# Performance work log

Hardware: AMD Instinct MI355X
Metric: run time of the kernel (lower is better)

## Reference

```python
import jax, jax.numpy as jnp
import numpy as np

B, N, D, H = 8, 1024, 1024, 16
DH = D // H
EPS = 1e-5


def setup_inputs() -> dict:
    key = jax.random.key(0)
    ks = jax.random.split(key, 12)
    s = 0.02
    return {
        "k": jax.random.normal(ks[0], (B, N, D), jnp.float32),
        "q": jax.random.normal(ks[1], (B, N, D), jnp.float32),
        "r": jax.random.normal(ks[2], (B, N, D), jnp.float32),
        "Wk": jax.random.normal(ks[3], (D, D), jnp.float32) * s,
        "bk": jnp.zeros((D,), jnp.float32),
        "Wq": jax.random.normal(ks[4], (D, D), jnp.float32) * s,
        "bq": jnp.zeros((D,), jnp.float32),
        "Wv": jax.random.normal(ks[5], (D, D), jnp.float32) * s,
        "bv": jnp.zeros((D,), jnp.float32),
        "Wo": jax.random.normal(ks[6], (D, D), jnp.float32) * s,
        "bo": jnp.zeros((D,), jnp.float32),
        "g1": jnp.ones((D,), jnp.float32),
        "b1": jnp.zeros((D,), jnp.float32),
        "g2": jnp.ones((D,), jnp.float32),
        "b2": jnp.zeros((D,), jnp.float32),
    }


def _layer_norm(x, g, b):
    mu = jnp.mean(x, axis=-1, keepdims=True)
    var = jnp.mean(jnp.square(x - mu), axis=-1, keepdims=True)
    return (x - mu) * jax.lax.rsqrt(var + EPS) * g + b


def reference(k, q, r, Wk, bk, Wq, bq, Wv, bv, Wo, bo, g1, b1, g2, b2):
    # linear projections (torch Linear: x @ W.T + b)
    kh = (k @ Wk.T + bk).reshape(B, -1, H, DH).transpose(0, 2, 1, 3)  # [B,H,Nk,DH]
    qh = (q @ Wq.T + bq).reshape(B, -1, H, DH).transpose(0, 2, 1, 3)  # [B,H,Nq,DH]
    vh = (r @ Wv.T + bv).reshape(B, -1, H, DH).transpose(0, 2, 1, 3)  # [B,H,Nk,DH]
    scale = 1.0 / jnp.sqrt(jnp.float32(DH))
    scores = jnp.einsum('bhid,bhjd->bhij', qh, kh) * scale  # [B,H,Nq,Nk]
    attn = jax.nn.softmax(scores, axis=-1)
    o = jnp.einsum('bhij,bhjd->bhid', attn, vh)  # [B,H,Nq,DH]
    o = o.transpose(0, 2, 1, 3).reshape(B, -1, D)
    mha = o @ Wo.T + bo
    residual = _layer_norm(mha + q, g1, b1)
    # source bug: mlp = nn.ReLU(BatchLinear(...)) -> mlp is plain ReLU
    out = _layer_norm(jax.nn.relu(residual) + residual, g2, b2)
    return out
```

## Files before the change

kernel.cpp:

```cpp
#include <hip/hip_runtime.h>
#include <hip/hip_bf16.h>
#include <math.h>

#define BB 8
#define NN 1024
#define DD 1024
#define HH 16
#define DH 64
#define MTOK 8192

typedef __attribute__((ext_vector_type(8))) short short8;
typedef __attribute__((ext_vector_type(4))) short short4v;
typedef __attribute__((ext_vector_type(4))) float float4v;

__device__ __forceinline__ ushort f2bf(float f) {
    union { float f; unsigned u; } v; v.f = f;
    unsigned r = v.u + 0x7fffu + ((v.u >> 16) & 1u);
    return (ushort)(r >> 16);
}

__device__ __forceinline__ void gl_lds16(const ushort* g, ushort* l) {
    __builtin_amdgcn_global_load_lds(
        (const __attribute__((address_space(1))) void*)g,
        (__attribute__((address_space(3))) void*)l, 16, 0, 0);
}

__device__ __forceinline__ void stage8f(const float* __restrict__ p, ushort* d) {
    float4v a = *(const float4v*)p;
    float4v b = *(const float4v*)(p + 4);
    short8 s;
    s[0]=(short)f2bf(a[0]); s[1]=(short)f2bf(a[1]); s[2]=(short)f2bf(a[2]); s[3]=(short)f2bf(a[3]);
    s[4]=(short)f2bf(b[0]); s[5]=(short)f2bf(b[1]); s[6]=(short)f2bf(b[2]); s[7]=(short)f2bf(b[3]);
    *(short8*)d = s;
}

struct CvtArgs {
    const float* src[7];
    ushort* dst[7];
    int n[7];
};
__global__ __launch_bounds__(256) void cvt_bf16(CvtArgs a) {
    const int z = blockIdx.y;
    const int idx = (blockIdx.x * 256 + threadIdx.x) * 8;
    if (idx >= a.n[z]) return;
    const float* s = a.src[z];
    float4v x0 = *(const float4v*)(s + idx);
    float4v x1 = *(const float4v*)(s + idx + 4);
    short8 o;
    o[0]=(short)f2bf(x0[0]); o[1]=(short)f2bf(x0[1]); o[2]=(short)f2bf(x0[2]); o[3]=(short)f2bf(x0[3]);
    o[4]=(short)f2bf(x1[0]); o[5]=(short)f2bf(x1[1]); o[6]=(short)f2bf(x1[2]); o[7]=(short)f2bf(x1[3]);
    *(short8*)(a.dst[z] + idx) = o;
}

template <typename TA, typename TW, int MODE>
__device__ __forceinline__ void gemm_core(const void* Ap, const void* Wp,
                                          const float* __restrict__ bias,
                                          void* __restrict__ outp,
                                          ushort* As, ushort* Bs) {
    constexpr bool A_BF = (sizeof(TA) == 2);
    constexpr bool W_BF = (sizeof(TW) == 2);
    constexpr int LDA = A_BF ? 64 : 72;
    constexpr int LDB = W_BF ? 64 : 72;

    const int tid  = threadIdx.x;
    const int wid  = tid >> 6;
    const int lane = tid & 63;
    const int quad = lane >> 4;
    const int l15  = lane & 15;
    const int wr   = wid >> 1;
    const int wc   = wid & 1;
    const int m0   = blockIdx.x * 128;
    const int n0   = blockIdx.y * 128;
    const int sw   = l15 & 7;

    float4v acc[4][4] = {};

    for (int kt = 0; kt < 16; ++kt) {
        const int k0 = kt * 64;
        if constexpr (A_BF) {
            const ushort* A = (const ushort*)Ap;
            #pragma unroll
            for (int t = 0; t < 4; ++t) {
                int chunk = t * 4 + wid;
                int row   = chunk * 8 + (lane >> 3);
                int kc    = ((lane & 7) ^ (lane >> 3)) * 8;
                gl_lds16(A + (size_t)(m0 + row) * 1024 + k0 + kc, As + chunk * 512);
            }
        } else {
            const float* A = (const float*)Ap;
            #pragma unroll
            for (int i = 0; i < 4; ++i) {
                int cidx = i * 256 + tid;
                int row  = cidx >> 3;
                int kc   = (cidx & 7) * 8;
                stage8f(A + (size_t)(m0 + row) * 1024 + k0 + kc, &As[row * 72 + kc]);
            }
        }
        if constexpr (W_BF) {
            const ushort* W = (const ushort*)Wp;
            #pragma unroll
            for (int t = 0; t < 4; ++t) {
                int chunk = t * 4 + wid;
                int row   = chunk * 8 + (lane >> 3);
                int kc    = ((lane & 7) ^ (lane >> 3)) * 8;
                gl_lds16(W + (size_t)(n0 + row) * 1024 + k0 + kc, Bs + chunk * 512);
            }
        } else {
            const float* W = (const float*)Wp;
            #pragma unroll
            for (int i = 0; i < 4; ++i) {
                int cidx = i * 256 + tid;
                int row  = cidx >> 3;
                int kc   = (cidx & 7) * 8;
                stage8f(W + (size_t)(n0 + row) * 1024 + k0 + kc, &Bs[row * 72 + kc]);
            }
        }
        __syncthreads();

        #pragma unroll
        for (int kk = 0; kk < 2; ++kk) {
            short8 af[4], bfr[4];
            #pragma unroll
            for (int i = 0; i < 4; ++i)
                af[i] = *(const short8*)&As[(wr * 64 + i * 16 + l15) * LDA +
                        (A_BF ? (((kk * 4 + quad) ^ sw) * 8) : (kk * 32 + quad * 8))];
            #pragma unroll
            for (int j = 0; j < 4; ++j)
                bfr[j] = *(const short8*)&Bs[(wc * 64 + j * 16 + l15) * LDB +
                         (W_BF ? (((kk * 4 + quad) ^ sw) * 8) : (kk * 32 + quad * 8))];
            #pragma unroll
            for (int i = 0; i < 4; ++i)
                #pragma unroll
                for (int j = 0; j < 4; ++j) {
                    if constexpr (MODE == 1)
                        acc[i][j] = __builtin_amdgcn_mfma_f32_16x16x32_bf16(af[i], bfr[j], acc[i][j], 0, 0, 0);
                    else
                        acc[j][i] = __builtin_amdgcn_mfma_f32_16x16x32_bf16(bfr[j], af[i], acc[j][i], 0, 0, 0);
                }
        }
        __syncthreads();
    }

    if constexpr (MODE == 1) {
        ushort* out = (ushort*)outp;
        #pragma unroll
        for (int j = 0; j < 4; ++j) {
            const int col = n0 + wc * 64 + j * 16 + l15;
            const float bv = bias[col];
            const int h = col >> 6;
            const int d = col & 63;
            #pragma unroll
            for (int i = 0; i < 4; ++i) {
                const int rowbase = m0 + wr * 64 + i * 16 + quad * 4;
                int bi = rowbase >> 10, n = rowbase & 1023;
                short4v pk;
                #pragma unroll
                for (int r = 0; r < 4; ++r) pk[r] = (short)f2bf(acc[i][j][r] + bv);
                *(short4v*)&out[(((size_t)(bi * HH + h) * DH + d) * NN) + n] = pk;
            }
        }
    } else {
        #pragma unroll
        for (int p = 0; p < 4; ++p) {
            const int fb = n0 + wc * 64 + p * 16 + quad * 4;
            const float4v bv4 = *(const float4v*)&bias[fb];
            const int h = fb >> 6;
            const int d = fb & 63;
            #pragma unroll
            for (int q = 0; q < 4; ++q) {
                const int tok = m0 + wr * 64 + q * 16 + l15;
                if constexpr (MODE == 0) {
                    ushort* out = (ushort*)outp;
                    int bi = tok >> 10, n = tok & 1023;
                    short4v pk;
                    #pragma unroll
                    for (int r = 0; r < 4; ++r) pk[r] = (short)f2bf(acc[p][q][r] + bv4[r]);
                    *(short4v*)&out[(((size_t)(bi * HH + h) * NN + n) * DH) + d] = pk;
                } else {
                    float* out = (float*)outp;
                    float4v ov;
                    #pragma unroll
                    for (int r = 0; r < 4; ++r) ov[r] = acc[p][q][r] + bv4[r];
                    *(float4v*)&out[(size_t)tok * 1024 + fb] = ov;
                }
            }
        }
    }
}

template <typename TA, typename TW>
__global__ __launch_bounds__(256) void proj3(const void* q, const void* k, const void* r,
                                             const void* Wq, const void* Wk, const void* Wv,
                                             const float* bq, const float* bk, const float* bv,
                                             ushort* qh, ushort* kh, ushort* vt) {
    constexpr int SA = (sizeof(TA) == 2) ? 64 : 72;
    constexpr int SB = (sizeof(TW) == 2) ? 64 : 72;
    __shared__ ushort As[128 * SA];
    __shared__ ushort Bs[128 * SB];
    if (blockIdx.z == 0)      gemm_core<TA, TW, 0>(q, Wq, bq, qh, As, Bs);
    else if (blockIdx.z == 1) gemm_core<TA, TW, 0>(k, Wk, bk, kh, As, Bs);
    else                      gemm_core<TA, TW, 1>(r, Wv, bv, vt, As, Bs);
}

template <typename TA, typename TW>
__global__ __launch_bounds__(256) void gemm_out(const void* A, const void* W,
                                                const float* bias, float* out) {
    constexpr int SA = (sizeof(TA) == 2) ? 64 : 72;
    constexpr int SB = (sizeof(TW) == 2) ? 64 : 72;
    __shared__ ushort As[128 * SA];
    __shared__ ushort Bs[128 * SB];
    gemm_core<TA, TW, 2>(A, W, bias, out, As, Bs);
}

__global__ __launch_bounds__(256) void attn_fused(const ushort* __restrict__ qh,
                                                  const ushort* __restrict__ kh,
                                                  const ushort* __restrict__ vt,
                                                  ushort* __restrict__ o) {
    __shared__ ushort Ks[64 * 64];
    __shared__ ushort Vs[64 * 64];
    __shared__ ushort Ps[4][2][16 * 72];

    const int tid  = threadIdx.x;
    const int wid  = tid >> 6;
    const int lane = tid & 63;
    const int quad = lane >> 4;
    const int l15  = lane & 15;
    const int sw   = l15 & 7;
    const int bh   = blockIdx.x;
    const int qt   = blockIdx.y;
    const int h    = bh & 15;
    const int b    = bh >> 4;

    const ushort* qb = qh + (size_t)bh * NN * DH;
    const ushort* kb = kh + (size_t)bh * NN * DH;
    const ushort* vb = vt + (size_t)bh * DH * NN;

    short8 qf[2][2];
    #pragma unroll
    for (int u = 0; u < 2; ++u) {
        const int qrow = qt * 128 + wid * 32 + u * 16 + l15;
        qf[u][0] = *(const short8*)(qb + (size_t)qrow * DH + quad * 8);
        qf[u][1] = *(const short8*)(qb + (size_t)qrow * DH + 32 + quad * 8);
    }

    float lsum[2] = {0.f, 0.f};
    float4v oaccT[2][4] = {};
    const float SCL = 0.18033688011f;

    for (int kt = 0; kt < 16; ++kt) {
        #pragma unroll
        for (int t = 0; t < 2; ++t) {
            int chunk = t * 4 + wid;
            int row   = chunk * 8 + (lane >> 3);
            int kc    = ((lane & 7) ^ (lane >> 3)) * 8;
            gl_lds16(kb + (size_t)(kt * 64 + row) * DH + kc, Ks + chunk * 512);
            gl_lds16(vb + (size_t)row * NN + kt * 64 + kc, Vs + chunk * 512);
        }
        __syncthreads();

        float4v sacc[2][4] = {};
        #pragma unroll
        for (int s = 0; s < 2; ++s)
            #pragma unroll
            for (int c = 0; c < 4; ++c) {
                short8 kf = *(const short8*)&Ks[(c * 16 + l15) * 64 + ((s * 4 + quad) ^ sw) * 8];
                #pragma unroll
                for (int u = 0; u < 2; ++u)
                    sacc[u][c] = __builtin_amdgcn_mfma_f32_16x16x32_bf16(kf, qf[u][s], sacc[u][c], 0, 0, 0);
            }

        #pragma unroll
        for (int u = 0; u < 2; ++u)
            #pragma unroll
            for (int c = 0; c < 4; ++c) {
                short4v pk;
                #pragma unroll
                for (int rr = 0; rr < 4; ++rr) {
                    float p = exp2f(sacc[u][c][rr] * SCL);
                    lsum[u] += p;
                    pk[rr] = (short)f2bf(p);
                }
                *(short4v*)&Ps[wid][u][l15 * 72 + c * 16 + quad * 4] = pk;
            }

        #pragma unroll
        for (int s = 0; s < 2; ++s) {
            short8 pf[2];
            #pragma unroll
            for (int u = 0; u < 2; ++u)
                pf[u] = *(const short8*)&Ps[wid][u][l15 * 72 + s * 32 + quad * 8];
            #pragma unroll
            for (int nn = 0; nn < 4; ++nn) {
                short8 vf = *(const short8*)&Vs[(nn * 16 + l15) * 64 + ((s * 4 + quad) ^ sw) * 8];
                #pragma unroll
                for (int u = 0; u < 2; ++u)
                    oaccT[u][nn] = __builtin_amdgcn_mfma_f32_16x16x32_bf16(vf, pf[u], oaccT[u][nn], 0, 0, 0);
            }
        }
        __syncthreads();
    }

    #pragma unroll
    for (int u = 0; u < 2; ++u) {
        float t = lsum[u];
        t += __shfl_xor(t, 16);
        t += __shfl_xor(t, 32);
        float inv = 1.0f / t;
        int row = qt * 128 + wid * 32 + u * 16 + l15;
        size_t base = ((size_t)b * NN + row) * DD + h * 64 + quad * 4;
        #pragma unroll
        for (int nn = 0; nn < 4; ++nn) {
            short4v pk;
            #pragma unroll
            for (int rr = 0; rr < 4; ++rr) pk[rr] = (short)f2bf(oaccT[u][nn][rr] * inv);
            *(short4v*)&o[base + nn * 16] = pk;
        }
    }
}

__global__ __launch_bounds__(256) void ln_fuse(const float* __restrict__ mha,
                                               const float* __restrict__ q,
                                               const float* __restrict__ g1,
                                               const float* __restrict__ b1,
                                               const float* __restrict__ g2,
                                               const float* __restrict__ b2,
                                               float* __restrict__ out) {
    __shared__ float red1[8];
    __shared__ float red2[8];
    const int tid  = threadIdx.x;
    const int wid  = tid >> 6;
    const int lane = tid & 63;
    const size_t base = (size_t)blockIdx.x * 1024 + tid * 4;

    float4v xv = *(const float4v*)(mha + base);
    float4v qv = *(const float4v*)(q + base);
    float x[4];
    float s = 0.f, ss = 0.f;
    for (int i = 0; i < 4; ++i) {
        x[i] = xv[i] + qv[i];
        s += x[i]; ss += x[i] * x[i];
    }
    for (int off = 1; off < 64; off <<= 1) {
        s += __shfl_xor(s, off); ss += __shfl_xor(ss, off);
    }
    if (lane == 0) { red1[wid * 2] = s; red1[wid * 2 + 1] = ss; }
    __syncthreads();
    s  = red1[0] + red1[2] + red1[4] + red1[6];
    ss = red1[1] + red1[3] + red1[5] + red1[7];
    float mu = s * (1.0f / 1024.0f);
    float rstd = rsqrtf(ss * (1.0f / 1024.0f) - mu * mu + 1e-5f);

    float4v g1v = *(const float4v*)(g1 + tid * 4);
    float4v b1v = *(const float4v*)(b1 + tid * 4);
    float y[4];
    float s2 = 0.f, ss2 = 0.f;
    for (int i = 0; i < 4; ++i) {
        float rr = (x[i] - mu) * rstd * g1v[i] + b1v[i];
        y[i] = fmaxf(rr, 0.f) + rr;
        s2 += y[i]; ss2 += y[i] * y[i];
    }
    for (int off = 1; off < 64; off <<= 1) {
        s2 += __shfl_xor(s2, off); ss2 += __shfl_xor(ss2, off);
    }
    if (lane == 0) { red2[wid * 2] = s2; red2[wid * 2 + 1] = ss2; }
    __syncthreads();
    s2  = red2[0] + red2[2] + red2[4] + red2[6];
    ss2 = red2[1] + red2[3] + red2[5] + red2[7];
    float mu2 = s2 * (1.0f / 1024.0f);
    float rstd2 = rsqrtf(ss2 * (1.0f / 1024.0f) - mu2 * mu2 + 1e-5f);

    float4v g2v = *(const float4v*)(g2 + tid * 4);
    float4v b2v = *(const float4v*)(b2 + tid * 4);
    float4v ov;
    for (int i = 0; i < 4; ++i) ov[i] = (y[i] - mu2) * rstd2 * g2v[i] + b2v[i];
    *(float4v*)(out + base) = ov;
}

extern "C" void kernel_launch(void* const* d_in, const int* in_sizes, int n_in,
                              void* d_out, int out_size, void* d_ws, size_t ws_size,
                              hipStream_t stream) {
    const float* k  = (const float*)d_in[0];
    const float* q  = (const float*)d_in[1];
    const float* r  = (const float*)d_in[2];
    const float* Wk = (const float*)d_in[3];
    const float* bk = (const float*)d_in[4];
    const float* Wq = (const float*)d_in[5];
    const float* bq = (const float*)d_in[6];
    const float* Wv = (const float*)d_in[7];
    const float* bv = (const float*)d_in[8];
    const float* Wo = (const float*)d_in[9];
    const float* bo = (const float*)d_in[10];
    const float* g1 = (const float*)d_in[11];
    const float* b1 = (const float*)d_in[12];
    const float* g2 = (const float*)d_in[13];
    const float* b2 = (const float*)d_in[14];

    char* ws = (char*)d_ws;
    const size_t MB = 1u << 20;
    dim3 blk(256);

    if (ws_size >= 121 * MB) {
        ushort* qc  = (ushort*)(ws);
        ushort* kc  = (ushort*)(ws + 16 * MB);
        ushort* rc  = (ushort*)(ws + 32 * MB);
        ushort* Wqc = (ushort*)(ws + 48 * MB);
        ushort* Wkc = (ushort*)(ws + 50 * MB);
        ushort* Wvc = (ushort*)(ws + 52 * MB);
        ushort* Woc = (ushort*)(ws + 54 * MB);
        ushort* qh  = (ushort*)(ws + 56 * MB);
        ushort* kh  = (ushort*)(ws + 72 * MB);
        ushort* vt  = (ushort*)(ws + 88 * MB);
        ushort* ob  = (ushort*)(ws + 104 * MB);
        float*  mh  = (float*)(ws);

        CvtArgs ca;
        ca.src[0] = q;  ca.dst[0] = qc;  ca.n[0] = MTOK * DD;
        ca.src[1] = k;  ca.dst[1] = kc;  ca.n[1] = MTOK * DD;
        ca.src[2] = r;  ca.dst[2] = rc;  ca.n[2] = MTOK * DD;
        ca.src[3] = Wq; ca.dst[3] = Wqc; ca.n[3] = DD * DD;
        ca.src[4] = Wk; ca.dst[4] = Wkc; ca.n[4] = DD * DD;
        ca.src[5] = Wv; ca.dst[5] = Wvc; ca.n[5] = DD * DD;
        ca.src[6] = Wo; ca.dst[6] = Woc; ca.n[6] = DD * DD;
        cvt_bf16<<<dim3(4096, 7), blk, 0, stream>>>(ca);

        proj3<ushort, ushort><<<dim3(64, 8, 3), blk, 0, stream>>>(
            qc, kc, rc, Wqc, Wkc, Wvc, bq, bk, bv, qh, kh, vt);
        attn_fused<<<dim3(HH * BB, 8), blk, 0, stream>>>(qh, kh, vt, ob);
        gemm_out<ushort, ushort><<<dim3(64, 8), blk, 0, stream>>>(ob, Woc, bo, mh);
        ln_fuse<<<dim3(MTOK), blk, 0, stream>>>(mh, q, g1, b1, g2, b2, (float*)d_out);
    } else {
        ushort* qh  = (ushort*)(ws);
        ushort* kh  = (ushort*)(ws + 16 * MB);
        ushort* vt  = (ushort*)(ws + 32 * MB);
        ushort* ob  = (ushort*)(ws + 48 * MB);
        ushort* Wqc = (ushort*)(ws + 48 * MB);
        ushort* Wkc = (ushort*)(ws + 50 * MB);
        ushort* Wvc = (ushort*)(ws + 52 * MB);
        float*  mh  = (float*)(ws);

        CvtArgs ca;
        ca.src[0] = Wq; ca.dst[0] = Wqc; ca.n[0] = DD * DD;
        ca.src[1] = Wk; ca.dst[1] = Wkc; ca.n[1] = DD * DD;
        ca.src[2] = Wv; ca.dst[2] = Wvc; ca.n[2] = DD * DD;
        for (int i = 3; i < 7; ++i) { ca.src[i] = Wq; ca.dst[i] = Wqc; ca.n[i] = 0; }
        cvt_bf16<<<dim3(512, 3), blk, 0, stream>>>(ca);

        proj3<float, ushort><<<dim3(64, 8, 3), blk, 0, stream>>>(
            q, k, r, Wqc, Wkc, Wvc, bq, bk, bv, qh, kh, vt);
        attn_fused<<<dim3(HH * BB, 8), blk, 0, stream>>>(qh, kh, vt, ob);
        gemm_out<ushort, float><<<dim3(64, 8), blk, 0, stream>>>(ob, Wo, bo, mh);
        ln_fuse<<<dim3(MTOK), blk, 0, stream>>>(mh, q, g1, b1, g2, b2, (float*)d_out);
    }
}
```

Measured before the change: 353.2 us.

## Fuse activation bf16 conversion into projection GEMM staging and prescale Q

Drops the separate pass that converted the q, k and r activations to bf16. The projection GEMM now loads fp32 activations and converts them while staging into LDS, using the same XOR-swizzled 64-wide layout as the bf16 path. The softmax scale is folded into the Q projection epilogue, which removes a multiply per score in attention. bf16 packing switches to a perm-based round-half-up helper, trading exact round-to-nearest-even for fewer instructions. The cost is register-staged fp32 loads in the GEMM main loop instead of async global-to-LDS copies for A.

```diff
diff --git a/kernel.cpp b/kernel.cpp
--- a/kernel.cpp
+++ b/kernel.cpp
@@ -13,25 +13,32 @@
 typedef __attribute__((ext_vector_type(4))) short short4v;
 typedef __attribute__((ext_vector_type(4))) float float4v;
 
+#define SCL_Q 0.18033688011112042f
+
 __device__ __forceinline__ ushort f2bf(float f) {
     union { float f; unsigned u; } v; v.f = f;
     unsigned r = v.u + 0x7fffu + ((v.u >> 16) & 1u);
     return (ushort)(r >> 16);
 }
 
+__device__ __forceinline__ unsigned pkbf2(float a, float b) {
+    union { float f; unsigned u; } x, y; x.f = a; y.f = b;
+    return __builtin_amdgcn_perm(y.u + 0x8000u, x.u + 0x8000u, 0x07060302u);
+}
+
 __device__ __forceinline__ void gl_lds16(const ushort* g, ushort* l) {
     __builtin_amdgcn_global_load_lds(
         (const __attribute__((address_space(1))) void*)g,
         (__attribute__((address_space(3))) void*)l, 16, 0, 0);
 }
 
-__device__ __forceinline__ void stage8f(const float* __restrict__ p, ushort* d) {
+__device__ __forceinline__ void stage8f_sw(const float* __restrict__ p, ushort* d) {
     float4v a = *(const float4v*)p;
     float4v b = *(const float4v*)(p + 4);
-    short8 s;
-    s[0]=(short)f2bf(a[0]); s[1]=(short)f2bf(a[1]); s[2]=(short)f2bf(a[2]); s[3]=(short)f2bf(a[3]);
-    s[4]=(short)f2bf(b[0]); s[5]=(short)f2bf(b[1]); s[6]=(short)f2bf(b[2]); s[7]=(short)f2bf(b[3]);
-    *(short8*)d = s;
+    uint4 w;
+    w.x = pkbf2(a[0], a[1]); w.y = pkbf2(a[2], a[3]);
+    w.z = pkbf2(b[0], b[1]); w.w = pkbf2(b[2], b[3]);
+    *(uint4*)d = w;
 }
 
 struct CvtArgs {
@@ -55,12 +62,10 @@
 template <typename TA, typename TW, int MODE>
 __device__ __forceinline__ void gemm_core(const void* Ap, const void* Wp,
                                           const float* __restrict__ bias,
-                                          void* __restrict__ outp,
+                                          void* __restrict__ outp, float oscale,
                                           ushort* As, ushort* Bs) {
     constexpr bool A_BF = (sizeof(TA) == 2);
     constexpr bool W_BF = (sizeof(TW) == 2);
-    constexpr int LDA = A_BF ? 64 : 72;
-    constexpr int LDB = W_BF ? 64 : 72;
 
     const int tid  = threadIdx.x;
     const int wid  = tid >> 6;
@@ -92,8 +97,10 @@
             for (int i = 0; i < 4; ++i) {
                 int cidx = i * 256 + tid;
                 int row  = cidx >> 3;
-                int kc   = (cidx & 7) * 8;
-                stage8f(A + (size_t)(m0 + row) * 1024 + k0 + kc, &As[row * 72 + kc]);
+                int cc   = cidx & 7;
+                int swc  = cc ^ (row & 7);
+                stage8f_sw(A + (size_t)(m0 + row) * 1024 + k0 + cc * 8,
+                           &As[row * 64 + swc * 8]);
             }
         }
         if constexpr (W_BF) {
@@ -111,8 +118,10 @@
             for (int i = 0; i < 4; ++i) {
                 int cidx = i * 256 + tid;
                 int row  = cidx >> 3;
-                int kc   = (cidx & 7) * 8;
-                stage8f(W + (size_t)(n0 + row) * 1024 + k0 + kc, &Bs[row * 72 + kc]);
+                int cc   = cidx & 7;
+                int swc  = cc ^ (row & 7);
+                stage8f_sw(W + (size_t)(n0 + row) * 1024 + k0 + cc * 8,
+                           &Bs[row * 64 + swc * 8]);
             }
         }
         __syncthreads();
@@ -122,12 +131,12 @@
             short8 af[4], bfr[4];
             #pragma unroll
             for (int i = 0; i < 4; ++i)
-                af[i] = *(const short8*)&As[(wr * 64 + i * 16 + l15) * LDA +
-                        (A_BF ? (((kk * 4 + quad) ^ sw) * 8) : (kk * 32 + quad * 8))];
+                af[i] = *(const short8*)&As[(wr * 64 + i * 16 + l15) * 64 +
+                                            ((kk * 4 + quad) ^ sw) * 8];
             #pragma unroll
             for (int j = 0; j < 4; ++j)
-                bfr[j] = *(const short8*)&Bs[(wc * 64 + j * 16 + l15) * LDB +
-                         (W_BF ? (((kk * 4 + quad) ^ sw) * 8) : (kk * 32 + quad * 8))];
+                bfr[j] = *(const short8*)&Bs[(wc * 64 + j * 16 + l15) * 64 +
+                                             ((kk * 4 + quad) ^ sw) * 8];
             #pragma unroll
             for (int i = 0; i < 4; ++i)
                 #pragma unroll
@@ -153,10 +162,10 @@
             for (int i = 0; i < 4; ++i) {
                 const int rowbase = m0 + wr * 64 + i * 16 + quad * 4;
                 int bi = rowbase >> 10, n = rowbase & 1023;
-                short4v pk;
-                #pragma unroll
-                for (int r = 0; r < 4; ++r) pk[r] = (short)f2bf(acc[i][j][r] + bv);
-                *(short4v*)&out[(((size_t)(bi * HH + h) * DH + d) * NN) + n] = pk;
+                uint2 w;
+                w.x = pkbf2(acc[i][j][0] + bv, acc[i][j][1] + bv);
+                w.y = pkbf2(acc[i][j][2] + bv, acc[i][j][3] + bv);
+                *(uint2*)&out[(((size_t)(bi * HH + h) * DH + d) * NN) + n] = w;
             }
         }
     } else {
@@ -172,10 +181,12 @@
                 if constexpr (MODE == 0) {
                     ushort* out = (ushort*)outp;
                     int bi = tok >> 10, n = tok & 1023;
-                    short4v pk;
-                    #pragma unroll
-                    for (int r = 0; r < 4; ++r) pk[r] = (short)f2bf(acc[p][q][r] + bv4[r]);
-                    *(short4v*)&out[(((size_t)(bi * HH + h) * NN + n) * DH) + d] = pk;
+                    uint2 w;
+                    w.x = pkbf2((acc[p][q][0] + bv4[0]) * oscale,
+                                (acc[p][q][1] + bv4[1]) * oscale);
+                    w.y = pkbf2((acc[p][q][2] + bv4[2]) * oscale,
+                                (acc[p][q][3] + bv4[3]) * oscale);
+                    *(uint2*)&out[(((size_t)(bi * HH + h) * NN + n) * DH) + d] = w;
                 } else {
                     float* out = (float*)outp;
                     float4v ov;
@@ -193,23 +204,19 @@
                                              const void* Wq, const void* Wk, const void* Wv,
                                              const float* bq, const float* bk, const float* bv,
                                              ushort* qh, ushort* kh, ushort* vt) {
-    constexpr int SA = (sizeof(TA) == 2) ? 64 : 72;
-    constexpr int SB = (sizeof(TW) == 2) ? 64 : 72;
-    __shared__ ushort As[128 * SA];
-    __shared__ ushort Bs[128 * SB];
-    if (blockIdx.z == 0)      gemm_core<TA, TW, 0>(q, Wq, bq, qh, As, Bs);
-    else if (blockIdx.z == 1) gemm_core<TA, TW, 0>(k, Wk, bk, kh, As, Bs);
-    else                      gemm_core<TA, TW, 1>(r, Wv, bv, vt, As, Bs);
+    __shared__ ushort As[128 * 64];
+    __shared__ ushort Bs[128 * 64];
+    if (blockIdx.z == 0)      gemm_core<TA, TW, 0>(q, Wq, bq, qh, SCL_Q, As, Bs);
+    else if (blockIdx.z == 1) gemm_core<TA, TW, 0>(k, Wk, bk, kh, 1.0f, As, Bs);
+    else                      gemm_core<TA, TW, 1>(r, Wv, bv, vt, 1.0f, As, Bs);
 }
 
 template <typename TA, typename TW>
 __global__ __launch_bounds__(256) void gemm_out(const void* A, const void* W,
                                                 const float* bias, float* out) {
-    constexpr int SA = (sizeof(TA) == 2) ? 64 : 72;
-    constexpr int SB = (sizeof(TW) == 2) ? 64 : 72;
-    __shared__ ushort As[128 * SA];
-    __shared__ ushort Bs[128 * SB];
-    gemm_core<TA, TW, 2>(A, W, bias, out, As, Bs);
+    __shared__ ushort As[128 * 64];
+    __shared__ ushort Bs[128 * 64];
+    gemm_core<TA, TW, 2>(A, W, bias, out, 1.0f, As, Bs);
 }
 
 __global__ __launch_bounds__(256) void attn_fused(const ushort* __restrict__ qh,
@@ -245,7 +252,6 @@
 
     float lsum[2] = {0.f, 0.f};
     float4v oaccT[2][4] = {};
-    const float SCL = 0.18033688011f;
 
     for (int kt = 0; kt < 16; ++kt) {
         #pragma unroll
@@ -273,14 +279,15 @@
         for (int u = 0; u < 2; ++u)
             #pragma unroll
             for (int c = 0; c < 4; ++c) {
-                short4v pk;
-                #pragma unroll
-                for (int rr = 0; rr < 4; ++rr) {
-                    float p = exp2f(sacc[u][c][rr] * SCL);
-                    lsum[u] += p;
-                    pk[rr] = (short)f2bf(p);
-                }
-                *(short4v*)&Ps[wid][u][l15 * 72 + c * 16 + quad * 4] = pk;
+                float p0 = exp2f(sacc[u][c][0]);
+                float p1 = exp2f(sacc[u][c][1]);
+                float p2 = exp2f(sacc[u][c][2]);
+                float p3 = exp2f(sacc[u][c][3]);
+                lsum[u] += (p0 + p1) + (p2 + p3);
+                uint2 w;
+                w.x = pkbf2(p0, p1);
+                w.y = pkbf2(p2, p3);
+                *(uint2*)&Ps[wid][u][l15 * 72 + c * 16 + quad * 4] = w;
             }
 
         #pragma unroll
@@ -310,10 +317,10 @@
         size_t base = ((size_t)b * NN + row) * DD + h * 64 + quad * 4;
         #pragma unroll
         for (int nn = 0; nn < 4; ++nn) {
-            short4v pk;
-            #pragma unroll
-            for (int rr = 0; rr < 4; ++rr) pk[rr] = (short)f2bf(oaccT[u][nn][rr] * inv);
-            *(short4v*)&o[base + nn * 16] = pk;
+            uint2 w;
+            w.x = pkbf2(oaccT[u][nn][0] * inv, oaccT[u][nn][1] * inv);
+            w.y = pkbf2(oaccT[u][nn][2] * inv, oaccT[u][nn][3] * inv);
+            *(uint2*)&o[base + nn * 16] = w;
         }
     }
 }
@@ -399,32 +406,27 @@
     const size_t MB = 1u << 20;
     dim3 blk(256);
 
-    if (ws_size >= 121 * MB) {
-        ushort* qc  = (ushort*)(ws);
-        ushort* kc  = (ushort*)(ws + 16 * MB);
-        ushort* rc  = (ushort*)(ws + 32 * MB);
-        ushort* Wqc = (ushort*)(ws + 48 * MB);
-        ushort* Wkc = (ushort*)(ws + 50 * MB);
-        ushort* Wvc = (ushort*)(ws + 52 * MB);
-        ushort* Woc = (ushort*)(ws + 54 * MB);
-        ushort* qh  = (ushort*)(ws + 56 * MB);
-        ushort* kh  = (ushort*)(ws + 72 * MB);
-        ushort* vt  = (ushort*)(ws + 88 * MB);
-        ushort* ob  = (ushort*)(ws + 104 * MB);
+    if (ws_size >= 73 * MB) {
+        ushort* qh  = (ushort*)(ws);
+        ushort* kh  = (ushort*)(ws + 16 * MB);
+        ushort* vt  = (ushort*)(ws + 32 * MB);
+        ushort* ob  = (ushort*)(ws + 48 * MB);
+        ushort* Wqc = (ushort*)(ws + 64 * MB);
+        ushort* Wkc = (ushort*)(ws + 66 * MB);
+        ushort* Wvc = (ushort*)(ws + 68 * MB);
+        ushort* Woc = (ushort*)(ws + 70 * MB);
         float*  mh  = (float*)(ws);
 
         CvtArgs ca;
-        ca.src[0] = q;  ca.dst[0] = qc;  ca.n[0] = MTOK * DD;
-        ca.src[1] = k;  ca.dst[1] = kc;  ca.n[1] = MTOK * DD;
-        ca.src[2] = r;  ca.dst[2] = rc;  ca.n[2] = MTOK * DD;
-        ca.src[3] = Wq; ca.dst[3] = Wqc; ca.n[3] = DD * DD;
-        ca.src[4] = Wk; ca.dst[4] = Wkc; ca.n[4] = DD * DD;
-        ca.src[5] = Wv; ca.dst[5] = Wvc; ca.n[5] = DD * DD;
-        ca.src[6] = Wo; ca.dst[6] = Woc; ca.n[6] = DD * DD;
-        cvt_bf16<<<dim3(4096, 7), blk, 0, stream>>>(ca);
-
-        proj3<ushort, ushort><<<dim3(64, 8, 3), blk, 0, stream>>>(
-            qc, kc, rc, Wqc, Wkc, Wvc, bq, bk, bv, qh, kh, vt);
+        ca.src[0] = Wq; ca.dst[0] = Wqc; ca.n[0] = DD * DD;
+        ca.src[1] = Wk; ca.dst[1] = Wkc; ca.n[1] = DD * DD;
+        ca.src[2] = Wv; ca.dst[2] = Wvc; ca.n[2] = DD * DD;
+        ca.src[3] = Wo; ca.dst[3] = Woc; ca.n[3] = DD * DD;
+        for (int i = 4; i < 7; ++i) { ca.src[i] = Wq; ca.dst[i] = Wqc; ca.n[i] = 0; }
+        cvt_bf16<<<dim3(512, 4), blk, 0, stream>>>(ca);
+
+        proj3<float, ushort><<<dim3(64, 8, 3), blk, 0, stream>>>(
+            q, k, r, Wqc, Wkc, Wvc, bq, bk, bv, qh, kh, vt);
         attn_fused<<<dim3(HH * BB, 8), blk, 0, stream>>>(qh, kh, vt, ob);
         gemm_out<ushort, ushort><<<dim3(64, 8), blk, 0, stream>>>(ob, Woc, bo, mh);
         ln_fuse<<<dim3(MTOK), blk, 0, stream>>>(mh, q, g1, b1, g2, b2, (float*)d_out);
```

After: 367.8 us. 1.04x slower.
